# Optimization experiments

Measured on AMD Instinct MI355X. Metric: run time of the kernel, lower is better.

The kernel has to match this reference:

```python
import jax, jax.numpy as jnp
import numpy as np

KERNEL_SIZE = 10
CHANNELS = 3
MEAN = (KERNEL_SIZE - 1) // 2  # 4


def setup_inputs() -> dict:
    key = jax.random.key(0)
    x = jax.random.uniform(key, (32, CHANNELS, 512, 512), dtype=jnp.float32)
    return {"x": x}


def reference(x) -> jnp.ndarray:
    # (1 - x) * 0.5, then replicate pad by MEAN on H and W
    y = (1.0 - x) * 0.5
    y = jnp.pad(y, ((0, 0), (0, 0), (MEAN, MEAN), (MEAN, MEAN)), mode="edge")
    # depthwise (groups=channels) conv with all-ones 10x10 kernel, VALID padding
    # weight layout OIHW with O=CHANNELS, I=1 (feature_group_count=CHANNELS)
    w = jnp.ones((CHANNELS, 1, KERNEL_SIZE, KERNEL_SIZE), dtype=x.dtype)
    out = jax.lax.conv_general_dilated(
        y, w,
        window_strides=(1, 1),
        padding="VALID",
        dimension_numbers=("NCHW", "OIHW", "NCHW"),
        feature_group_count=CHANNELS,
    )
    return out  # [B, C, H-1, W-1]
```

## Files before the change

kernel.cpp:

```cpp
#include <hip/hip_runtime.h>


#define IMG 512
#define OUTW 511
#define KS 10
#define MEAN 4
#define SUBB 16
#define ROWF4 (IMG / 4)
#define NTHREADS 1024
#define NBANDS (IMG / SUBB)
#define NIMG 96
#define NWG (NBANDS * NIMG)
#define CPX (NWG / 8)

__device__ __forceinline__ float4 f4add(float4 a, float4 b) {
    return make_float4(a.x + b.x, a.y + b.y, a.z + b.z, a.w + b.w);
}

__global__ __launch_bounds__(NTHREADS, 8) void onedilate_kernel(
    const float* __restrict__ x, float* __restrict__ out)
{
    __shared__ float Vb[SUBB * IMG];

    const int lin = blockIdx.y * NBANDS + blockIdx.x;
    const int swz = (lin & 7) * CPX + (lin >> 3);
    const int bx  = swz & (NBANDS - 1);
    const int bc  = swz >> 5;

    const int tid = threadIdx.x;
    const int jc  = tid & (ROWF4 - 1);
    const int rg  = tid >> 7;
    const int rb  = bx * SUBB;

    const float* __restrict__ xim = x + (size_t)bc * (IMG * IMG);
    float* __restrict__ oim = out + (size_t)bc * (OUTW * OUTW);

    {
        const int i0 = rb + 2 * rg;
        const float* cp = xim + jc * 4;
#define TROW(k_) (*(const float4*)(cp + (size_t)min(max(i0 - MEAN + (k_), 0), IMG - 1) * IMG))
        const float4 t0  = TROW(0);
        const float4 t1  = TROW(1);
        const float4 t2  = TROW(2);
        const float4 t3  = TROW(3);
        const float4 t4  = TROW(4);
        const float4 t5  = TROW(5);
        const float4 t6  = TROW(6);
        const float4 t7  = TROW(7);
        const float4 t8  = TROW(8);
        const float4 t9  = TROW(9);
        const float4 t10 = TROW(10);
#undef TROW
        const float4 s01 = f4add(t0, t1), s23 = f4add(t2, t3);
        const float4 s45 = f4add(t4, t5), s67 = f4add(t6, t7);
        const float4 s89 = f4add(t8, t9);
        const float4 v0 = f4add(f4add(f4add(s01, s23), f4add(s45, s67)), s89);
        const float4 v1 = make_float4(v0.x + t10.x - t0.x, v0.y + t10.y - t0.y,
                                      v0.z + t10.z - t0.z, v0.w + t10.w - t0.w);
        float4* Vv = (float4*)Vb;
        Vv[(2 * rg + 0) * ROWF4 + jc] = v0;
        Vv[(2 * rg + 1) * ROWF4 + jc] = v1;
    }
    __syncthreads();

    const int cbase = 4 * jc;
    const int bl0 = max(cbase - 4, 0);
    const int bl2 = min(cbase + 4, IMG - 4);
    const int bl3 = min(cbase + 8, IMG - 4);
    const bool lo0 = (cbase - 4 < 0);
    const bool hi2 = (cbase + 4 > IMG - 4);
    const bool hi3 = (cbase + 8 > IMG - 4);

#pragma unroll
    for (int k = 0; k < 2; ++k) {
        const int r = 2 * rg + k;
        const float* rp = Vb + r * IMG;
        float4 v0 = *(const float4*)(rp + bl0);
        float4 v1 = *(const float4*)(rp + cbase);
        float4 v2 = *(const float4*)(rp + bl2);
        float4 v3 = *(const float4*)(rp + bl3);
        if (lo0) v0 = make_float4(v0.x, v0.x, v0.x, v0.x);
        if (hi2) v2 = make_float4(v2.w, v2.w, v2.w, v2.w);
        const float w12 = hi3 ? v3.w : v3.x;

        const float S = ((v0.x + v0.y) + (v0.z + v0.w))
                      + ((v1.x + v1.y) + (v1.z + v1.w))
                      + (v2.x + v2.y);
        const float d1  = v2.z - v0.x;
        const float d2  = v2.w - v0.y;
        const float d3  = w12  - v0.z;
        const float d12 = d1 + d2;

        const int i = rb + r;
        if (i < OUTW) {
            float* op = oim + (size_t)i * OUTW + cbase;
            op[0] = fmaf(S, -0.5f, 50.0f);
            op[1] = fmaf(S + d1, -0.5f, 50.0f);
            op[2] = fmaf(S + d12, -0.5f, 50.0f);
            if (cbase + 3 < OUTW)
                op[3] = fmaf(S + (d12 + d3), -0.5f, 50.0f);
        }
    }
}

extern "C" void kernel_launch(void* const* d_in, const int* in_sizes, int n_in,
                              void* d_out, int out_size, void* d_ws, size_t ws_size,
                              hipStream_t stream) {
    const float* x = (const float*)d_in[0];
    float* out = (float*)d_out;

    dim3 block(NTHREADS, 1, 1);
    dim3 grid(NBANDS, NIMG, 1);
    onedilate_kernel<<<grid, block, 0, stream>>>(x, out);
}
```

Before: 181.6 us.

## Halve row band per workgroup, add unclamped load path, vectorize output stores

Shrinks each workgroup to 8 output rows with 512 threads, adjusting the image swizzle to match. Interior bands now load their 11 input rows without per-row clamping, with a scheduling barrier placed after the loads. Output rows are written as float4 stores where possible instead of scalar stores. The smaller bands add occupancy and more workgroups but also more redundant halo reads. The float4 stores are not 16-byte aligned because the row stride is 511, so they rely on unaligned global access being allowed and may be slower.

```diff
diff --git a/kernel.cpp b/kernel.cpp
--- a/kernel.cpp
+++ b/kernel.cpp
@@ -5,9 +5,9 @@
 #define OUTW 511
 #define KS 10
 #define MEAN 4
-#define SUBB 16
+#define SUBB 8
 #define ROWF4 (IMG / 4)
-#define NTHREADS 1024
+#define NTHREADS 512
 #define NBANDS (IMG / SUBB)
 #define NIMG 96
 #define NWG (NBANDS * NIMG)
@@ -17,7 +17,7 @@
     return make_float4(a.x + b.x, a.y + b.y, a.z + b.z, a.w + b.w);
 }
 
-__global__ __launch_bounds__(NTHREADS, 8) void onedilate_kernel(
+__global__ __launch_bounds__(NTHREADS, 4) void onedilate_kernel(
     const float* __restrict__ x, float* __restrict__ out)
 {
     __shared__ float Vb[SUBB * IMG];
@@ -25,7 +25,7 @@
     const int lin = blockIdx.y * NBANDS + blockIdx.x;
     const int swz = (lin & 7) * CPX + (lin >> 3);
     const int bx  = swz & (NBANDS - 1);
-    const int bc  = swz >> 5;
+    const int bc  = swz >> 6;
 
     const int tid = threadIdx.x;
     const int jc  = tid & (ROWF4 - 1);
@@ -38,25 +38,28 @@
     {
         const int i0 = rb + 2 * rg;
         const float* cp = xim + jc * 4;
-#define TROW(k_) (*(const float4*)(cp + (size_t)min(max(i0 - MEAN + (k_), 0), IMG - 1) * IMG))
-        const float4 t0  = TROW(0);
-        const float4 t1  = TROW(1);
-        const float4 t2  = TROW(2);
-        const float4 t3  = TROW(3);
-        const float4 t4  = TROW(4);
-        const float4 t5  = TROW(5);
-        const float4 t6  = TROW(6);
-        const float4 t7  = TROW(7);
-        const float4 t8  = TROW(8);
-        const float4 t9  = TROW(9);
-        const float4 t10 = TROW(10);
-#undef TROW
-        const float4 s01 = f4add(t0, t1), s23 = f4add(t2, t3);
-        const float4 s45 = f4add(t4, t5), s67 = f4add(t6, t7);
-        const float4 s89 = f4add(t8, t9);
+        float4 t[11];
+        if (rb >= MEAN && rb + 12 <= IMG - 1) {
+            const float* p = cp + (size_t)(i0 - MEAN) * IMG;
+#pragma unroll
+            for (int k = 0; k < 11; ++k)
+                t[k] = *(const float4*)(p + (size_t)k * IMG);
+        } else {
+#pragma unroll
+            for (int k = 0; k < 11; ++k) {
+                const int ri = min(max(i0 - MEAN + k, 0), IMG - 1);
+                t[k] = *(const float4*)(cp + (size_t)ri * IMG);
+            }
+        }
+        __builtin_amdgcn_sched_barrier(0);
+
+        const float4 s01 = f4add(t[0], t[1]), s23 = f4add(t[2], t[3]);
+        const float4 s45 = f4add(t[4], t[5]), s67 = f4add(t[6], t[7]);
+        const float4 s89 = f4add(t[8], t[9]);
         const float4 v0 = f4add(f4add(f4add(s01, s23), f4add(s45, s67)), s89);
-        const float4 v1 = make_float4(v0.x + t10.x - t0.x, v0.y + t10.y - t0.y,
-                                      v0.z + t10.z - t0.z, v0.w + t10.w - t0.w);
+        const float4 v1 = make_float4(
+            v0.x + t[10].x - t[0].x, v0.y + t[10].y - t[0].y,
+            v0.z + t[10].z - t[0].z, v0.w + t[10].w - t[0].w);
         float4* Vv = (float4*)Vb;
         Vv[(2 * rg + 0) * ROWF4 + jc] = v0;
         Vv[(2 * rg + 1) * ROWF4 + jc] = v1;
@@ -94,11 +97,17 @@
         const int i = rb + r;
         if (i < OUTW) {
             float* op = oim + (size_t)i * OUTW + cbase;
-            op[0] = fmaf(S, -0.5f, 50.0f);
-            op[1] = fmaf(S + d1, -0.5f, 50.0f);
-            op[2] = fmaf(S + d12, -0.5f, 50.0f);
-            if (cbase + 3 < OUTW)
-                op[3] = fmaf(S + (d12 + d3), -0.5f, 50.0f);
+            const float4 o = make_float4(fmaf(S, -0.5f, 50.0f),
+                                         fmaf(S + d1, -0.5f, 50.0f),
+                                         fmaf(S + d12, -0.5f, 50.0f),
+                                         fmaf(S + (d12 + d3), -0.5f, 50.0f));
+            if (cbase + 3 < OUTW) {
+                *(float4*)op = o;
+            } else {
+                op[0] = o.x;
+                op[1] = o.y;
+                op[2] = o.z;
+            }
         }
     }
 }
```

New measurement: 258.1 us. 1.42x slower.
